# Kernel tuning notes

Hardware: AMD Instinct MI355X
Metric: run time of the kernel (lower is better)

Reference implementation:

```python
import jax, jax.numpy as jnp
import numpy as np

N_QUBITS = 4
N_FEATURES = 16
B = 1048576


def _bcast(theta):
    # theta: scalar or [B]; make broadcastable against [B,2,2,2] amp slices
    return theta if jnp.ndim(theta) == 0 else theta.reshape(theta.shape[0], 1, 1, 1)


def apply_ry(state, theta, w):
    # state: [B,2,2,2,2] complex; RY(theta) on wire w
    th = _bcast(theta)
    c = jnp.cos(th / 2).astype(state.dtype)
    s = jnp.sin(th / 2).astype(state.dtype)
    st = jnp.moveaxis(state, w + 1, -1)
    a0, a1 = st[..., 0], st[..., 1]
    st = jnp.stack([c * a0 - s * a1, s * a0 + c * a1], axis=-1)
    return jnp.moveaxis(st, -1, w + 1)


def apply_rz(state, theta, w):
    # RZ(theta) = diag(e^{-i theta/2}, e^{+i theta/2}) on wire w
    th = _bcast(theta)
    ph = jnp.exp(-0.5j * th.astype(jnp.float32)).astype(state.dtype)
    st = jnp.moveaxis(state, w + 1, -1)
    a0, a1 = st[..., 0], st[..., 1]
    st = jnp.stack([ph * a0, jnp.conj(ph) * a1], axis=-1)
    return jnp.moveaxis(st, -1, w + 1)


def cnot(state, c, t):
    st = jnp.moveaxis(state, (c + 1, t + 1), (-2, -1))  # [...,2(ctrl),2(tgt)]
    st = jnp.stack([st[..., 0, :], st[..., 1, ::-1]], axis=-2)
    return jnp.moveaxis(st, (-2, -1), (c + 1, t + 1))


def quantum_encoder_batched(x, qw):
    # x: [B,16] float32, qw: [8] float32 -> latents [B,4] (PauliZ expvals)
    b = x.shape[0]
    state = jnp.zeros((b, 16), jnp.complex64).at[:, 0].set(1.0)
    state = state.reshape(b, 2, 2, 2, 2)
    pi = jnp.float32(np.pi)
    for i in range(N_QUBITS):
        state = apply_ry(state, x[:, i] * pi, i)
        state = apply_rz(state, x[:, i + N_QUBITS] * pi, i)
    for i in range(N_QUBITS - 1):
        state = cnot(state, i, i + 1)
    for i in range(N_QUBITS):
        state = apply_ry(state, qw[2 * i], i)
        state = apply_rz(state, qw[2 * i + 1], i)
    for i in range(N_QUBITS - 1):
        state = cnot(state, i, i + 1)
    probs = state.real ** 2 + state.imag ** 2  # [B,2,2,2,2]
    zs = []
    for i in range(N_QUBITS):
        axes = tuple(a for a in range(1, N_QUBITS + 1) if a != i + 1)
        p = probs.sum(axes)  # [B,2]
        zs.append(p[:, 0] - p[:, 1])
    return jnp.stack(zs, axis=1)  # [B,4]


def setup_inputs() -> dict:
    key = jax.random.key(0)
    ks = jax.random.split(key, 8)
    x = jax.random.uniform(ks[0], (B, N_FEATURES), dtype=jnp.float32)
    q_weights = 0.01 * jax.random.normal(ks[1], (2 * N_QUBITS,), dtype=jnp.float32)
    # decoder: Linear(4,16) -> ReLU -> Linear(16,32) -> ReLU -> Linear(32,16)
    W1 = jax.random.normal(ks[2], (16, 4), dtype=jnp.float32) / jnp.sqrt(4.0)
    b1 = jnp.zeros((16,), jnp.float32)
    W2 = jax.random.normal(ks[3], (32, 16), dtype=jnp.float32) / jnp.sqrt(16.0)
    b2 = jnp.zeros((32,), jnp.float32)
    W3 = jax.random.normal(ks[4], (16, 32), dtype=jnp.float32) / jnp.sqrt(32.0)
    b3 = jnp.zeros((16,), jnp.float32)
    return {"x": x, "q_weights": q_weights, "W1": W1, "b1": b1,
            "W2": W2, "b2": b2, "W3": W3, "b3": b3}


def reference(x, q_weights, W1, b1, W2, b2, W3, b3):
    z = quantum_encoder_batched(x, q_weights)          # [B,4]
    h = jax.nn.relu(z @ W1.T + b1)                      # [B,16]
    h = jax.nn.relu(h @ W2.T + b2)                      # [B,32]
    return h @ W3.T + b3                                # [B,16]
```

## Files before the change

### kernel.cpp

```cpp
#include <hip/hip_runtime.h>

using u16 = unsigned short;
using u32 = unsigned int;
typedef float f32x4 __attribute__((ext_vector_type(4)));
typedef short s16x8 __attribute__((ext_vector_type(8)));

union FragU { u32 d[4]; s16x8 s; uint4 q; };

__device__ __forceinline__ u32 cvt_pk_bf16(float a, float b) {
    u32 r;
    asm("v_cvt_pk_bf16_f32 %0, %1, %2" : "=v"(r) : "v"(a), "v"(b));
    return r;
}
__device__ __forceinline__ void split2(float w0, float w1, u32& hi, u32& lo) {
    u32 u0 = __float_as_uint(w0), u1 = __float_as_uint(w1);
    hi = (u0 >> 16) | (u1 & 0xFFFF0000u);
    float r0 = w0 - __uint_as_float(u0 & 0xFFFF0000u);
    float r1 = w1 - __uint_as_float(u1 & 0xFFFF0000u);
    lo = cvt_pk_bf16(r0, r1);
}
__device__ __forceinline__ u32 bp(int ib, u32 v) {
    return (u32)__builtin_amdgcn_ds_bpermute(ib, (int)v);
}
__device__ __forceinline__ f32x4 tov(float4 v) { return (f32x4){v.x, v.y, v.z, v.w}; }
#define MFMA16 __builtin_amdgcn_mfma_f32_16x16x32_bf16

__global__ void __launch_bounds__(256) qae_bperm(
    const float* __restrict__ x,  const float* __restrict__ qw,
    const float* __restrict__ W1, const float* __restrict__ b1,
    const float* __restrict__ W2, const float* __restrict__ b2,
    const float* __restrict__ W3, const float* __restrict__ b3,
    float* __restrict__ out, int n)
{
    int tid  = threadIdx.x;
    int b    = blockIdx.x * 256 + tid;
    int bc   = b < n ? b : n - 1;
    int lane = tid & 63;
    int vn   = lane & 15, vq = lane >> 4;
    int gbase = blockIdx.x * 256 + (tid - lane);

    const float4* xf = reinterpret_cast<const float4*>(x);
    float4 xa = xf[(size_t)bc * 4];
    float4 xc = xf[(size_t)bc * 4 + 1];

    float4 w1r = reinterpret_cast<const float4*>(W1)[vn];
    const float4* p0 = reinterpret_cast<const float4*>(W2 + vn * 16 + (vq & 1) * 8);
    float4 a0 = p0[0], a1 = p0[1];
    const float4* p1 = reinterpret_cast<const float4*>(W2 + (16 + vn) * 16 + (vq & 1) * 8);
    float4 c0 = p1[0], c1v = p1[1];
    const float4* p3 = reinterpret_cast<const float4*>(W3 + vn * 32 + vq * 8);
    float4 e0 = p3[0], e1 = p3[1];

    float4 c1b  = reinterpret_cast<const float4*>(b1)[vq];
    float4 c2b0 = reinterpret_cast<const float4*>(b2)[vq];
    float4 c2b1 = reinterpret_cast<const float4*>(b2)[4 + vq];
    float4 c3b  = reinterpret_cast<const float4*>(b3)[vq];

    bool q0 = (vq == 0), q1v = (vq == 1), qlt2 = (vq < 2);

    FragU A1, A2a, A2b, A3h, A3l;
    {
        u32 h0, l0, h1, l1; split2(w1r.x, w1r.y, h0, l0); split2(w1r.z, w1r.w, h1, l1);
        A1.d[0] = q0 ? h0 : (q1v ? l0 : 0);
        A1.d[1] = q0 ? h1 : (q1v ? l1 : 0);
        A1.d[2] = 0; A1.d[3] = 0;
        u32 h, l;
        split2(a0.x, a0.y, h, l);   A2a.d[0] = qlt2 ? h : l;
        split2(a0.z, a0.w, h, l);   A2a.d[1] = qlt2 ? h : l;
        split2(a1.x, a1.y, h, l);   A2a.d[2] = qlt2 ? h : l;
        split2(a1.z, a1.w, h, l);   A2a.d[3] = qlt2 ? h : l;
        split2(c0.x, c0.y, h, l);   A2b.d[0] = qlt2 ? h : l;
        split2(c0.z, c0.w, h, l);   A2b.d[1] = qlt2 ? h : l;
        split2(c1v.x, c1v.y, h, l); A2b.d[2] = qlt2 ? h : l;
        split2(c1v.z, c1v.w, h, l); A2b.d[3] = qlt2 ? h : l;
        split2(e0.x, e0.y, h, l);   A3h.d[0] = h; A3l.d[0] = l;
        split2(e0.z, e0.w, h, l);   A3h.d[1] = h; A3l.d[1] = l;
        split2(e1.x, e1.y, h, l);   A3h.d[2] = h; A3l.d[2] = l;
        split2(e1.z, e1.w, h, l);   A3h.d[3] = h; A3l.d[3] = l;
    }

    float th[4]  = { xa.x, xa.y, xa.z, xa.w };
    float phv[4] = { xc.x, xc.y, xc.z, xc.w };
    float Zb[4], Xb[4], Yb[4];
    #pragma unroll
    for (int i = 0; i < 4; ++i) {
        float ct = __builtin_amdgcn_cosf(th[i]  * 0.5f);
        float st = __builtin_amdgcn_sinf(th[i]  * 0.5f);
        float cp = __builtin_amdgcn_cosf(phv[i] * 0.5f);
        float sp = __builtin_amdgcn_sinf(phv[i] * 0.5f);
        Zb[i] = ct; Xb[i] = st * cp; Yb[i] = st * sp;
    }
    const float INV2PI = 0.15915494309189535f;
    float CA[4], SA[4];
    #pragma unroll
    for (int v = 0; v < 4; ++v) {
        float a = qw[2 * v] * INV2PI;
        CA[v] = __builtin_amdgcn_cosf(a);
        SA[v] = __builtin_amdgcn_sinf(a);
    }
    float K00 = CA[0]*CA[1], K10 = SA[0]*CA[1], K01 = CA[0]*SA[1], K11 = SA[0]*SA[1];
    float L00 = CA[2]*CA[3], L10 = SA[2]*CA[3], L01 = CA[2]*SA[3], L11 = SA[2]*SA[3];
    float X01 = Xb[0]*Xb[1], Y01 = Yb[0]*Yb[1];
    float X23 = Xb[2]*Xb[3], Y23 = Yb[2]*Yb[3];

    float zv0 = CA[0]*Zb[0] - SA[0]*X01;
    float zv1 = K00*Zb[1] - K01*(Zb[0]*Xb[1]*Xb[2]) + K10*Y01 + K11*(Xb[0]*Xb[2]);
    float t2a =  CA[2]*(Zb[0]*Zb[2])        - SA[2]*(Zb[1]*X23);
    float t2b = -CA[2]*(X01*Zb[2])          - SA[2]*(Y01*X23);
    float t2c =  CA[2]*(Yb[1]*Yb[2])        + SA[2]*(Zb[0]*Xb[1]*Xb[3]);
    float t2d = -CA[2]*(Yb[0]*Zb[1]*Yb[2])  - SA[2]*(Xb[0]*Xb[3]);
    float zv2 = K00*t2a + K10*t2b + K01*t2c + K11*t2d;
    float t3a =  L00*(Zb[1]*Zb[3])              + L10*(Zb[0]*Y23)
               - L01*(Zb[0]*Zb[2]*Xb[3])        + L11*(Zb[1]*Xb[2]);
    float t3b =  L00*(Y01*Zb[3])                - L10*(X01*Y23)
               + L01*(X01*Zb[2]*Xb[3])          + L11*(Y01*Xb[2]);
    float t3c = -L00*(Zb[0]*Xb[1]*Xb[2]*Zb[3])  - L10*(Yb[1]*Zb[2]*Yb[3])
               - L01*(Yb[1]*Yb[2]*Xb[3])        - L11*(Zb[0]*Xb[1]);
    float t3d =  L00*(Xb[0]*Xb[2]*Zb[3])        + L10*(Yb[0]*Zb[1]*Zb[2]*Yb[3])
               + L01*(Yb[0]*Zb[1]*Yb[2]*Xb[3])  + L11*Xb[0];
    float zv3 = K00*t3a + K10*t3b + K01*t3c + K11*t3d;

    u32 zd0 = cvt_pk_bf16(zv0, zv1);
    u32 zd1 = cvt_pk_bf16(zv2, zv3);

    int i2a = ((((2 * vq)    ) & 3) * 16 + vn) * 4;
    int i2b = ((((2 * vq) + 1) & 3) * 16 + vn) * 4;

    #pragma unroll
    for (int t = 0; t < 4; ++t) {
        int viL = (t * 16 + vn) * 4;
        FragU B1; B1.d[0] = bp(viL, zd0); B1.d[1] = bp(viL, zd1); B1.d[2] = 0; B1.d[3] = 0;
        f32x4 c1 = tov(c1b);
        c1 = MFMA16(A1.s, B1.s, c1, 0, 0, 0);
        u32 da0 = cvt_pk_bf16(fmaxf(c1[0], 0.f), fmaxf(c1[1], 0.f));
        u32 da1 = cvt_pk_bf16(fmaxf(c1[2], 0.f), fmaxf(c1[3], 0.f));

        FragU B2;
        B2.d[0] = bp(i2a, da0); B2.d[1] = bp(i2a, da1);
        B2.d[2] = bp(i2b, da0); B2.d[3] = bp(i2b, da1);
        f32x4 ca = tov(c2b0), cb = tov(c2b1);
        ca = MFMA16(A2a.s, B2.s, ca, 0, 0, 0);
        cb = MFMA16(A2b.s, B2.s, cb, 0, 0, 0);
        u32 ea0 = cvt_pk_bf16(fmaxf(ca[0],0.f), fmaxf(ca[1],0.f));
        u32 ea1 = cvt_pk_bf16(fmaxf(ca[2],0.f), fmaxf(ca[3],0.f));
        u32 eb0 = cvt_pk_bf16(fmaxf(cb[0],0.f), fmaxf(cb[1],0.f));
        u32 eb1 = cvt_pk_bf16(fmaxf(cb[2],0.f), fmaxf(cb[3],0.f));

        u32 s0a = bp(i2a, ea0), s0b = bp(i2a, eb0);
        u32 s1a = bp(i2a, ea1), s1b = bp(i2a, eb1);
        u32 s2_ = bp(i2b, ea0), s2b = bp(i2b, eb0);
        u32 s3a = bp(i2b, ea1), s3b = bp(i2b, eb1);
        FragU B3;
        B3.d[0] = qlt2 ? s0a : s0b;
        B3.d[1] = qlt2 ? s1a : s1b;
        B3.d[2] = qlt2 ? s2_ : s2b;
        B3.d[3] = qlt2 ? s3a : s3b;
        f32x4 c3 = tov(c3b);
        c3 = MFMA16(A3l.s, B3.s, c3, 0, 0, 0);
        c3 = MFMA16(A3h.s, B3.s, c3, 0, 0, 0);

        int R = gbase + t * 16 + vn;
        if (R < n)
            *reinterpret_cast<float4*>(out + (size_t)R * 16 + vq * 4) =
                make_float4(c3[0], c3[1], c3[2], c3[3]);
    }
}

extern "C" void kernel_launch(void* const* d_in, const int* in_sizes, int n_in,
                              void* d_out, int out_size, void* d_ws, size_t ws_size,
                              hipStream_t stream) {
    const float* x  = (const float*)d_in[0];
    const float* qw = (const float*)d_in[1];
    const float* W1 = (const float*)d_in[2];
    const float* b1 = (const float*)d_in[3];
    const float* W2 = (const float*)d_in[4];
    const float* b2 = (const float*)d_in[5];
    const float* W3 = (const float*)d_in[6];
    const float* b3 = (const float*)d_in[7];
    float* out = (float*)d_out;

    int n = in_sizes[0] / 16;
    int blocks = (n + 255) / 256;
    qae_bperm<<<blocks, 256, 0, stream>>>(x, qw, W1, b1, W2, b2, W3, b3, out, n);
}
```

Measured before the change: 126.2 us.

## Split encoder and MLP into two kernels via workspace buffer

Separates the closed-form quantum expectation computation into its own kernel that writes packed bf16 latents to the workspace, followed by an MLP kernel that reads them and runs the MFMA layers. Falls back to the original fused kernel when no workspace is available. This may reduce per-kernel register pressure and improve occupancy. The cost is an extra launch and an additional round trip of latents through global memory.

```diff
diff --git a/kernel.cpp b/kernel.cpp
--- a/kernel.cpp
+++ b/kernel.cpp
@@ -25,60 +25,9 @@
 __device__ __forceinline__ f32x4 tov(float4 v) { return (f32x4){v.x, v.y, v.z, v.w}; }
 #define MFMA16 __builtin_amdgcn_mfma_f32_16x16x32_bf16
 
-__global__ void __launch_bounds__(256) qae_bperm(
-    const float* __restrict__ x,  const float* __restrict__ qw,
-    const float* __restrict__ W1, const float* __restrict__ b1,
-    const float* __restrict__ W2, const float* __restrict__ b2,
-    const float* __restrict__ W3, const float* __restrict__ b3,
-    float* __restrict__ out, int n)
-{
-    int tid  = threadIdx.x;
-    int b    = blockIdx.x * 256 + tid;
-    int bc   = b < n ? b : n - 1;
-    int lane = tid & 63;
-    int vn   = lane & 15, vq = lane >> 4;
-    int gbase = blockIdx.x * 256 + (tid - lane);
-
-    const float4* xf = reinterpret_cast<const float4*>(x);
-    float4 xa = xf[(size_t)bc * 4];
-    float4 xc = xf[(size_t)bc * 4 + 1];
-
-    float4 w1r = reinterpret_cast<const float4*>(W1)[vn];
-    const float4* p0 = reinterpret_cast<const float4*>(W2 + vn * 16 + (vq & 1) * 8);
-    float4 a0 = p0[0], a1 = p0[1];
-    const float4* p1 = reinterpret_cast<const float4*>(W2 + (16 + vn) * 16 + (vq & 1) * 8);
-    float4 c0 = p1[0], c1v = p1[1];
-    const float4* p3 = reinterpret_cast<const float4*>(W3 + vn * 32 + vq * 8);
-    float4 e0 = p3[0], e1 = p3[1];
-
-    float4 c1b  = reinterpret_cast<const float4*>(b1)[vq];
-    float4 c2b0 = reinterpret_cast<const float4*>(b2)[vq];
-    float4 c2b1 = reinterpret_cast<const float4*>(b2)[4 + vq];
-    float4 c3b  = reinterpret_cast<const float4*>(b3)[vq];
-
-    bool q0 = (vq == 0), q1v = (vq == 1), qlt2 = (vq < 2);
-
-    FragU A1, A2a, A2b, A3h, A3l;
-    {
-        u32 h0, l0, h1, l1; split2(w1r.x, w1r.y, h0, l0); split2(w1r.z, w1r.w, h1, l1);
-        A1.d[0] = q0 ? h0 : (q1v ? l0 : 0);
-        A1.d[1] = q0 ? h1 : (q1v ? l1 : 0);
-        A1.d[2] = 0; A1.d[3] = 0;
-        u32 h, l;
-        split2(a0.x, a0.y, h, l);   A2a.d[0] = qlt2 ? h : l;
-        split2(a0.z, a0.w, h, l);   A2a.d[1] = qlt2 ? h : l;
-        split2(a1.x, a1.y, h, l);   A2a.d[2] = qlt2 ? h : l;
-        split2(a1.z, a1.w, h, l);   A2a.d[3] = qlt2 ? h : l;
-        split2(c0.x, c0.y, h, l);   A2b.d[0] = qlt2 ? h : l;
-        split2(c0.z, c0.w, h, l);   A2b.d[1] = qlt2 ? h : l;
-        split2(c1v.x, c1v.y, h, l); A2b.d[2] = qlt2 ? h : l;
-        split2(c1v.z, c1v.w, h, l); A2b.d[3] = qlt2 ? h : l;
-        split2(e0.x, e0.y, h, l);   A3h.d[0] = h; A3l.d[0] = l;
-        split2(e0.z, e0.w, h, l);   A3h.d[1] = h; A3l.d[1] = l;
-        split2(e1.x, e1.y, h, l);   A3h.d[2] = h; A3l.d[2] = l;
-        split2(e1.z, e1.w, h, l);   A3h.d[3] = h; A3l.d[3] = l;
-    }
-
+__device__ __forceinline__ void closed_form_z(
+    float4 xa, float4 xc, const float* __restrict__ qw, u32& zd0, u32& zd1)
+{
     float th[4]  = { xa.x, xa.y, xa.z, xa.w };
     float phv[4] = { xc.x, xc.y, xc.z, xc.w };
     float Zb[4], Xb[4], Yb[4];
@@ -120,9 +69,51 @@
                + L01*(Yb[0]*Zb[1]*Yb[2]*Xb[3])  + L11*Xb[0];
     float zv3 = K00*t3a + K10*t3b + K01*t3c + K11*t3d;
 
-    u32 zd0 = cvt_pk_bf16(zv0, zv1);
-    u32 zd1 = cvt_pk_bf16(zv2, zv3);
-
+    zd0 = cvt_pk_bf16(zv0, zv1);
+    zd1 = cvt_pk_bf16(zv2, zv3);
+}
+
+__device__ __forceinline__ void prep_frags(
+    const float* __restrict__ W1, const float* __restrict__ W2,
+    const float* __restrict__ W3, int vn, int vq,
+    FragU& A1, FragU& A2a, FragU& A2b, FragU& A3h, FragU& A3l)
+{
+    bool q0 = (vq == 0), q1v = (vq == 1), qlt2 = (vq < 2);
+    float4 w1r = reinterpret_cast<const float4*>(W1)[vn];
+    const float4* p0 = reinterpret_cast<const float4*>(W2 + vn * 16 + (vq & 1) * 8);
+    float4 a0 = p0[0], a1 = p0[1];
+    const float4* p1 = reinterpret_cast<const float4*>(W2 + (16 + vn) * 16 + (vq & 1) * 8);
+    float4 c0 = p1[0], c1v = p1[1];
+    const float4* p3 = reinterpret_cast<const float4*>(W3 + vn * 32 + vq * 8);
+    float4 e0 = p3[0], e1 = p3[1];
+
+    u32 h0, l0, h1, l1; split2(w1r.x, w1r.y, h0, l0); split2(w1r.z, w1r.w, h1, l1);
+    A1.d[0] = q0 ? h0 : (q1v ? l0 : 0);
+    A1.d[1] = q0 ? h1 : (q1v ? l1 : 0);
+    A1.d[2] = 0; A1.d[3] = 0;
+    u32 h, l;
+    split2(a0.x, a0.y, h, l);   A2a.d[0] = qlt2 ? h : l;
+    split2(a0.z, a0.w, h, l);   A2a.d[1] = qlt2 ? h : l;
+    split2(a1.x, a1.y, h, l);   A2a.d[2] = qlt2 ? h : l;
+    split2(a1.z, a1.w, h, l);   A2a.d[3] = qlt2 ? h : l;
+    split2(c0.x, c0.y, h, l);   A2b.d[0] = qlt2 ? h : l;
+    split2(c0.z, c0.w, h, l);   A2b.d[1] = qlt2 ? h : l;
+    split2(c1v.x, c1v.y, h, l); A2b.d[2] = qlt2 ? h : l;
+    split2(c1v.z, c1v.w, h, l); A2b.d[3] = qlt2 ? h : l;
+    split2(e0.x, e0.y, h, l);   A3h.d[0] = h; A3l.d[0] = l;
+    split2(e0.z, e0.w, h, l);   A3h.d[1] = h; A3l.d[1] = l;
+    split2(e1.x, e1.y, h, l);   A3h.d[2] = h; A3l.d[2] = l;
+    split2(e1.z, e1.w, h, l);   A3h.d[3] = h; A3l.d[3] = l;
+}
+
+__device__ __forceinline__ void mlp_tiles(
+    u32 zd0, u32 zd1, int vn, int vq, int gbase, int n,
+    const FragU& A1, const FragU& A2a, const FragU& A2b,
+    const FragU& A3h, const FragU& A3l,
+    float4 c1b, float4 c2b0, float4 c2b1, float4 c3b,
+    float* __restrict__ out)
+{
+    bool qlt2 = (vq < 2);
     int i2a = ((((2 * vq)    ) & 3) * 16 + vn) * 4;
     int i2b = ((((2 * vq) + 1) & 3) * 16 + vn) * 4;
 
@@ -166,6 +157,81 @@
     }
 }
 
+__global__ void __launch_bounds__(256) qae_encode(
+    const float* __restrict__ x, const float* __restrict__ qw,
+    uint2* __restrict__ zws, int n)
+{
+    int b = blockIdx.x * 256 + threadIdx.x;
+    int bc = b < n ? b : n - 1;
+    const float4* xf = reinterpret_cast<const float4*>(x);
+    float4 xa = xf[(size_t)bc * 4];
+    float4 xc = xf[(size_t)bc * 4 + 1];
+    u32 zd0, zd1;
+    closed_form_z(xa, xc, qw, zd0, zd1);
+    if (b < n) zws[b] = make_uint2(zd0, zd1);
+}
+
+__global__ void __launch_bounds__(256) qae_mlp(
+    const uint2* __restrict__ zws,
+    const float* __restrict__ W1, const float* __restrict__ b1,
+    const float* __restrict__ W2, const float* __restrict__ b2,
+    const float* __restrict__ W3, const float* __restrict__ b3,
+    float* __restrict__ out, int n)
+{
+    int tid  = threadIdx.x;
+    int b    = blockIdx.x * 256 + tid;
+    int bc   = b < n ? b : n - 1;
+    int lane = tid & 63;
+    int vn   = lane & 15, vq = lane >> 4;
+    int gbase = blockIdx.x * 256 + (tid - lane);
+
+    uint2 zd = zws[bc];
+
+    FragU A1, A2a, A2b, A3h, A3l;
+    prep_frags(W1, W2, W3, vn, vq, A1, A2a, A2b, A3h, A3l);
+
+    float4 c1b  = reinterpret_cast<const float4*>(b1)[vq];
+    float4 c2b0 = reinterpret_cast<const float4*>(b2)[vq];
+    float4 c2b1 = reinterpret_cast<const float4*>(b2)[4 + vq];
+    float4 c3b  = reinterpret_cast<const float4*>(b3)[vq];
+
+    mlp_tiles(zd.x, zd.y, vn, vq, gbase, n, A1, A2a, A2b, A3h, A3l,
+              c1b, c2b0, c2b1, c3b, out);
+}
+
+__global__ void __launch_bounds__(256) qae_bperm(
+    const float* __restrict__ x,  const float* __restrict__ qw,
+    const float* __restrict__ W1, const float* __restrict__ b1,
+    const float* __restrict__ W2, const float* __restrict__ b2,
+    const float* __restrict__ W3, const float* __restrict__ b3,
+    float* __restrict__ out, int n)
+{
+    int tid  = threadIdx.x;
+    int b    = blockIdx.x * 256 + tid;
+    int bc   = b < n ? b : n - 1;
+    int lane = tid & 63;
+    int vn   = lane & 15, vq = lane >> 4;
+    int gbase = blockIdx.x * 256 + (tid - lane);
+
+    const float4* xf = reinterpret_cast<const float4*>(x);
+    float4 xa = xf[(size_t)bc * 4];
+    float4 xc = xf[(size_t)bc * 4 + 1];
+
+    FragU A1, A2a, A2b, A3h, A3l;
+    prep_frags(W1, W2, W3, vn, vq, A1, A2a, A2b, A3h, A3l);
+
+    u32 zd0, zd1;
+    closed_form_z(xa, xc, qw, zd0, zd1);
+
+    float4 c1b  = reinterpret_cast<const float4*>(b1)[vq];
+    float4 c2b0 = reinterpret_cast<const float4*>(b2)[vq];
+    float4 c2b1 = reinterpret_cast<const float4*>(b2)[4 + vq];
+    float4 c3b  = reinterpret_cast<const float4*>(b3)[vq];
+
+    mlp_tiles(zd0, zd1, vn, vq, gbase, n, A1, A2a, A2b, A3h, A3l,
+              c1b, c2b0, c2b1, c3b, out);
+}
+
 extern "C" void kernel_launch(void* const* d_in, const int* in_sizes, int n_in,
                               void* d_out, int out_size, void* d_ws, size_t ws_size,
                               hipStream_t stream) {
@@ -181,5 +247,11 @@
 
     int n = in_sizes[0] / 16;
     int blocks = (n + 255) / 256;
-    qae_bperm<<<blocks, 256, 0, stream>>>(x, qw, W1, b1, W2, b2, W3, b3, out, n);
-}
+    if (d_ws != nullptr && ws_size >= (size_t)n * 8) {
+        uint2* zws = (uint2*)d_ws;
+        qae_encode<<<blocks, 256, 0, stream>>>(x, qw, zws, n);
+        qae_mlp<<<blocks, 256, 0, stream>>>(zws, W1, b1, W2, b2, W3, b3, out, n);
+    } else {
+        qae_bperm<<<blocks, 256, 0, stream>>>(x, qw, W1, b1, W2, b2, W3, b3, out, n);
+    }
+}
```

Result: slower. 131.9 us (+4.5%).
